# Kernel tuning notes

Measured on AMD Instinct MI355X. Metric: run time of the kernel, lower is better.

Reference implementation:

```python
import jax, jax.numpy as jnp
import numpy as np

B, T = 64, 2048
QD, KD, VD, AD = 512, 512, 512, 256


def setup_inputs() -> dict:
    key = jax.random.key(0)
    ks = jax.random.split(key, 9)
    s = lambda d: 1.0 / np.sqrt(d)
    return {
        "query": jax.random.normal(ks[0], (B, QD), jnp.float32),
        "key": jax.random.normal(ks[1], (B, T, KD), jnp.float32),
        "value": jax.random.normal(ks[2], (B, T, VD), jnp.float32),
        "Wq": jax.random.uniform(ks[3], (QD, AD), jnp.float32, -s(QD), s(QD)),
        "bq": jax.random.uniform(ks[4], (AD,), jnp.float32, -s(QD), s(QD)),
        "Wk": jax.random.uniform(ks[5], (KD, AD), jnp.float32, -s(KD), s(KD)),
        "bk": jax.random.uniform(ks[6], (AD,), jnp.float32, -s(KD), s(KD)),
        "Wo": jax.random.uniform(ks[7], (AD, 1), jnp.float32, -s(AD), s(AD)),
        "bo": jax.random.uniform(ks[8], (1,), jnp.float32, -s(AD), s(AD)),
    }


def reference(query, key, value, Wq, bq, Wk, bk, Wo, bo):
    # q_proj: [B, 1, AD]; k_proj: [B, T, AD]
    q_proj = (query @ Wq + bq)[:, None, :]
    k_proj = jnp.einsum("btk,ka->bta", key, Wk) + bk
    # score: [B, T, 1]
    score = jnp.tanh(q_proj + k_proj) @ Wo + bo
    attn = jax.nn.softmax(score, axis=1)  # softmax over keys (dim 1)
    # context: [B, VD] = sum_t attn[b,t] * value[b,t,:]
    context = jnp.einsum("bt,btv->bv", attn[..., 0], value)
    return context, attn[..., 0]
```

## Files before the change

### kernel.cpp

```cpp
#include <hip/hip_runtime.h>

#define NB 64
#define NT 2048
#define NQD 512
#define NKD 512
#define NVD 512
#define NAD 256

typedef __attribute__((ext_vector_type(8))) short s16x8;
typedef __attribute__((ext_vector_type(4))) float fx4;
typedef __attribute__((ext_vector_type(4))) unsigned int u32x4;

__device__ __forceinline__ short f2bf(float x) {
  union { float f; unsigned u; } v; v.f = x;
  return (short)((v.u + 0x7fffu + ((v.u >> 16) & 1u)) >> 16);
}

__device__ __forceinline__ unsigned cvt_pk_bf16(float lo, float hi) {
  unsigned r;
  asm("v_cvt_pk_bf16_f32 %0, %1, %2" : "=v"(r) : "v"(lo), "v"(hi));
  return r;
}

__device__ __forceinline__ float fast_tanh(float x) {
  float e = __expf(x + x);
  return 1.0f - 2.0f * __builtin_amdgcn_rcpf(e + 1.0f);
}

__device__ __forceinline__ void gload_lds16(const void* g, void* l) {
  __builtin_amdgcn_global_load_lds(
      (const __attribute__((address_space(1))) unsigned int*)g,
      (__attribute__((address_space(3))) unsigned int*)l, 16, 0, 0);
}

__global__ void prep_kernel(const float* __restrict__ query, const float* __restrict__ Wq,
                            const float* __restrict__ bq, const float* __restrict__ bk,
                            const float* __restrict__ Wk,
                            float* __restrict__ qpk, short* __restrict__ Bpk) {
  __shared__ float q[NQD];
  const int tid = threadIdx.x;
  if (blockIdx.x < NB) {
    const int b = blockIdx.x;
    for (int k = tid; k < NQD; k += 256) q[k] = query[b * NQD + k];
    __syncthreads();
    float acc = bq[tid] + bk[tid];
#pragma unroll 8
    for (int k = 0; k < NQD; ++k) acc += q[k] * Wq[k * NAD + tid];
    qpk[b * NAD + tid] = acc;
  } else {
    const int ks = blockIdx.x - NB;
#pragma unroll
    for (int rep = 0; rep < 4; ++rep) {
      const int o = rep * 256 + tid;
      const int wnt = o >> 6;
      const int l = o & 63;
      const int g = l >> 4, h = l & 15;
      const int n = wnt * 16 + h;
      const int k0 = ks * 32 + g * 8;
      s16x8 v;
#pragma unroll
      for (int j = 0; j < 8; ++j) v[j] = f2bf(Wk[(size_t)(k0 + j) * NAD + n]);
      *(s16x8*)(Bpk + (size_t)(ks * 1024 + o) * 8) = v;
    }
  }
}

__global__ void __launch_bounds__(512, 4)
score_kernel(const float* __restrict__ key, const short* __restrict__ Bpk,
             const float* __restrict__ qpk, const float* __restrict__ Wo,
             float* __restrict__ score) {
  __shared__ float As[2][128 * 32];
  __shared__ short Bs[2][256 * 32];
  __shared__ float sred[4][128];
  const int tid = threadIdx.x;
  const int W = tid >> 6, l = tid & 63;
  const int wr = W >> 2, wc = W & 3;
  const int g = l >> 4, h = l & 15;
  const int m0 = blockIdx.x * 128;
  const int b = m0 >> 11;

  const float* srcA[2];
  int loffA[2];
#pragma unroll
  for (int i = 0; i < 2; ++i) {
    const int p = W * 128 + i * 64 + l;
    const int row = p >> 3, c = p & 7;
    srcA[i] = key + (size_t)(m0 + row) * NKD + ((c ^ (row & 7)) << 2);
    loffA[i] = (W * 128 + i * 64) * 16;
  }
  const short* srcB[2];
  int loffB[2];
#pragma unroll
  for (int i = 0; i < 2; ++i) {
    const int o = W * 128 + i * 64 + l;
    srcB[i] = Bpk + (size_t)o * 8;
    loffB[i] = (W * 128 + i * 64) * 16;
  }

  auto stage = [&](int bb, int ck) {
#pragma unroll
    for (int i = 0; i < 2; ++i)
      gload_lds16(srcA[i] + ck * 32, (char*)&As[bb][0] + loffA[i]);
#pragma unroll
    for (int i = 0; i < 2; ++i)
      gload_lds16(srcB[i] + (size_t)ck * 8192, (char*)&Bs[bb][0] + loffB[i]);
  };

  stage(0, 0);
  stage(1, 1);

  fx4 acc[4][4];
#pragma unroll
  for (int i = 0; i < 4; ++i)
#pragma unroll
    for (int j = 0; j < 4; ++j) acc[i][j] = fx4{0.f, 0.f, 0.f, 0.f};

  for (int ck = 0; ck < 16; ++ck) {
    const int buf = ck & 1;
    if (ck < 15) asm volatile("s_waitcnt vmcnt(4)" ::: "memory");
    else         asm volatile("s_waitcnt vmcnt(0)" ::: "memory");
    __builtin_amdgcn_sched_barrier(0);
    __builtin_amdgcn_s_barrier();

    s16x8 bfr[4];
#pragma unroll
    for (int nt = 0; nt < 4; ++nt)
      bfr[nt] = *(const s16x8*)((const char*)&Bs[buf][0] + ((wc * 4 + nt) * 64 + l) * 16);
#pragma unroll
    for (int mt = 0; mt < 4; ++mt) {
      const int R = wr * 64 + mt * 16 + h;
      const char* base = (const char*)&As[buf][0] + R * 128;
      fx4 lo = *(const fx4*)(base + (((g * 2    ) ^ (R & 7)) << 4));
      fx4 hi = *(const fx4*)(base + (((g * 2 + 1) ^ (R & 7)) << 4));
      u32x4 uu;
      uu[0] = cvt_pk_bf16(lo[0], lo[1]);
      uu[1] = cvt_pk_bf16(lo[2], lo[3]);
      uu[2] = cvt_pk_bf16(hi[0], hi[1]);
      uu[3] = cvt_pk_bf16(hi[2], hi[3]);
      const s16x8 af = *(s16x8*)&uu;
#pragma unroll
      for (int nt = 0; nt < 4; ++nt)
        acc[mt][nt] = __builtin_amdgcn_mfma_f32_16x16x32_bf16(af, bfr[nt], acc[mt][nt], 0, 0, 0);
    }

    __builtin_amdgcn_s_barrier();
    if (ck < 14) stage(buf, ck + 2);
  }

  float qv[4], wv[4];
#pragma unroll
  for (int nt = 0; nt < 4; ++nt) {
    const int n = wc * 64 + nt * 16 + h;
    qv[nt] = qpk[b * NAD + n];
    wv[nt] = Wo[n];
  }
#pragma unroll
  for (int mt = 0; mt < 4; ++mt) {
#pragma unroll
    for (int rr = 0; rr < 4; ++rr) {
      float s = fast_tanh(acc[mt][0][rr] + qv[0]) * wv[0]
              + fast_tanh(acc[mt][1][rr] + qv[1]) * wv[1]
              + fast_tanh(acc[mt][2][rr] + qv[2]) * wv[2]
              + fast_tanh(acc[mt][3][rr] + qv[3]) * wv[3];
#pragma unroll
      for (int off = 1; off < 16; off <<= 1) s += __shfl_xor(s, off, 64);
      if (h == 0) sred[wc][wr * 64 + mt * 16 + g * 4 + rr] = s;
    }
  }
  __syncthreads();
  if (tid < 128)
    score[m0 + tid] = sred[0][tid] + sred[1][tid] + sred[2][tid] + sred[3][tid];
}

__global__ void ctx_sm_kernel(const float* __restrict__ score, const float* __restrict__ value,
                              float* __restrict__ attn, float* __restrict__ partial) {
  __shared__ float pa[NT];
  __shared__ float redm[4];
  __shared__ float reds[4];
  __shared__ fx4 red[128];
  const int blk = blockIdx.x;
  const int b = blk >> 5, tc = blk & 31;
  const int tid = threadIdx.x;

  const float* s = score + (size_t)b * NT;
  float v[8];
  float m = -3.0e38f;
#pragma unroll
  for (int j = 0; j < 8; ++j) { v[j] = s[tid + j * 256]; m = fmaxf(m, v[j]); }
#pragma unroll
  for (int off = 1; off < 64; off <<= 1) m = fmaxf(m, __shfl_xor(m, off, 64));
  if ((tid & 63) == 0) redm[tid >> 6] = m;
  __syncthreads();
  m = fmaxf(fmaxf(redm[0], redm[1]), fmaxf(redm[2], redm[3]));
  float sum = 0.f;
#pragma unroll
  for (int j = 0; j < 8; ++j) { v[j] = __expf(v[j] - m); sum += v[j]; }
#pragma unroll
  for (int off = 1; off < 64; off <<= 1) sum += __shfl_xor(sum, off, 64);
  if ((tid & 63) == 0) reds[tid >> 6] = sum;
  __syncthreads();
  sum = reds[0] + reds[1] + reds[2] + reds[3];
  const float inv = 1.0f / sum;
#pragma unroll
  for (int j = 0; j < 8; ++j) pa[tid + j * 256] = v[j] * inv;
  __syncthreads();

  if (tid < 64) attn[(size_t)b * NT + tc * 64 + tid] = pa[tc * 64 + tid];

  const float* a = &pa[tc * 64];
  const int half = tid >> 7;
  const int vi = (tid & 127) * 4;
  const float* vp = value + ((size_t)b * NT + tc * 64 + half) * NVD + vi;
  fx4 s4 = fx4{0.f, 0.f, 0.f, 0.f};
#pragma unroll 8
  for (int t = 0; t < 64; t += 2) {
    fx4 x = *(const fx4*)(vp + (size_t)t * NVD);
    s4 += x * a[t + half];
  }
  if (half) red[tid & 127] = s4;
  __syncthreads();
  if (!half) {
    s4 += red[tid];
    *(fx4*)(partial + (size_t)blk * NVD + vi) = s4;
  }
}

__global__ void ctx_reduce_kernel(const float* __restrict__ partial, float* __restrict__ ctx) {
  const int i = blockIdx.x * 256 + threadIdx.x;
  const int b = i >> 9, v = i & (NVD - 1);
  float s = 0.f;
#pragma unroll
  for (int tc = 0; tc < 32; ++tc) s += partial[(size_t)(b * 32 + tc) * NVD + v];
  ctx[i] = s;
}

extern "C" void kernel_launch(void* const* d_in, const int* in_sizes, int n_in,
                              void* d_out, int out_size, void* d_ws, size_t ws_size,
                              hipStream_t stream) {
  const float* query = (const float*)d_in[0];
  const float* key   = (const float*)d_in[1];
  const float* value = (const float*)d_in[2];
  const float* Wq    = (const float*)d_in[3];
  const float* bq    = (const float*)d_in[4];
  const float* Wk    = (const float*)d_in[5];
  const float* bk    = (const float*)d_in[6];
  const float* Wo    = (const float*)d_in[7];

  float* out  = (float*)d_out;
  float* ctx  = out;
  float* attn = out + NB * NVD;

  char* ws = (char*)d_ws;
  float* qpk     = (float*)(ws);
  short* Bpk     = (short*)(ws + 64 * 1024);
  float* score   = (float*)(ws + (64 + 256) * 1024);
  float* partial = (float*)(ws + (64 + 256 + 512) * 1024);

  prep_kernel<<<NB + 16, 256, 0, stream>>>(query, Wq, bq, bk, Wk, qpk, Bpk);
  score_kernel<<<(NB * NT) / 128, 512, 0, stream>>>(key, Bpk, qpk, Wo, score);
  ctx_sm_kernel<<<NB * 32, 256, 0, stream>>>(score, value, attn, partial);
  ctx_reduce_kernel<<<(NB * NVD) / 256, 256, 0, stream>>>(partial, ctx);
}
```

Measured before the change: 150.8 us.

## Split score GEMM columns across two smaller blocks with partial score buffers

The score kernel goes from 128x256 tiles on 512 threads to 64x128 tiles on 256 threads. Each pair of blocks covers the two column halves of the attention dimension, and each half writes its partial score to its own buffer. The softmax kernel sums the two partial buffers when it loads scores. This raises block count and should ease register and LDS pressure per block, but each key row is now loaded twice (by the two column-half blocks), relying on L2 to absorb the duplicate traffic.

```diff
diff --git a/kernel.cpp b/kernel.cpp
--- a/kernel.cpp
+++ b/kernel.cpp
@@ -65,18 +65,19 @@
   }
 }
 
-__global__ void __launch_bounds__(512, 4)
+__global__ void __launch_bounds__(256, 4)
 score_kernel(const float* __restrict__ key, const short* __restrict__ Bpk,
              const float* __restrict__ qpk, const float* __restrict__ Wo,
-             float* __restrict__ score) {
-  __shared__ float As[2][128 * 32];
-  __shared__ short Bs[2][256 * 32];
-  __shared__ float sred[4][128];
+             float* __restrict__ score0, float* __restrict__ score1) {
+  __shared__ float As[2][64 * 32];
+  __shared__ short Bs[2][128 * 32];
+  __shared__ float sred[4][64];
   const int tid = threadIdx.x;
   const int W = tid >> 6, l = tid & 63;
-  const int wr = W >> 2, wc = W & 3;
   const int g = l >> 4, h = l & 15;
-  const int m0 = blockIdx.x * 128;
+  const int bm = blockIdx.x >> 1;
+  const int bc = blockIdx.x & 1;
+  const int m0 = bm * 64;
   const int b = m0 >> 11;
 
   const float* srcA[2];
@@ -93,7 +94,7 @@
 #pragma unroll
   for (int i = 0; i < 2; ++i) {
     const int o = W * 128 + i * 64 + l;
-    srcB[i] = Bpk + (size_t)o * 8;
+    srcB[i] = Bpk + (size_t)bc * 4096 + (size_t)o * 8;
     loffB[i] = (W * 128 + i * 64) * 16;
   }
 
@@ -109,11 +110,11 @@
   stage(0, 0);
   stage(1, 1);
 
-  fx4 acc[4][4];
+  fx4 acc[4][2];
 #pragma unroll
   for (int i = 0; i < 4; ++i)
 #pragma unroll
-    for (int j = 0; j < 4; ++j) acc[i][j] = fx4{0.f, 0.f, 0.f, 0.f};
+    for (int j = 0; j < 2; ++j) acc[i][j] = fx4{0.f, 0.f, 0.f, 0.f};
 
   for (int ck = 0; ck < 16; ++ck) {
     const int buf = ck & 1;
@@ -122,13 +123,13 @@
     __builtin_amdgcn_sched_barrier(0);
     __builtin_amdgcn_s_barrier();
 
-    s16x8 bfr[4];
-#pragma unroll
-    for (int nt = 0; nt < 4; ++nt)
-      bfr[nt] = *(const s16x8*)((const char*)&Bs[buf][0] + ((wc * 4 + nt) * 64 + l) * 16);
+    s16x8 bfr[2];
+#pragma unroll
+    for (int nt = 0; nt < 2; ++nt)
+      bfr[nt] = *(const s16x8*)((const char*)&Bs[buf][0] + ((W * 2 + nt) * 64 + l) * 16);
 #pragma unroll
     for (int mt = 0; mt < 4; ++mt) {
-      const int R = wr * 64 + mt * 16 + h;
+      const int R = mt * 16 + h;
       const char* base = (const char*)&As[buf][0] + R * 128;
       fx4 lo = *(const fx4*)(base + (((g * 2    ) ^ (R & 7)) << 4));
       fx4 hi = *(const fx4*)(base + (((g * 2 + 1) ^ (R & 7)) << 4));
@@ -139,7 +140,7 @@
       uu[3] = cvt_pk_bf16(hi[2], hi[3]);
       const s16x8 af = *(s16x8*)&uu;
 #pragma unroll
-      for (int nt = 0; nt < 4; ++nt)
+      for (int nt = 0; nt < 2; ++nt)
         acc[mt][nt] = __builtin_amdgcn_mfma_f32_16x16x32_bf16(af, bfr[nt], acc[mt][nt], 0, 0, 0);
     }
 
@@ -147,10 +148,10 @@
     if (ck < 14) stage(buf, ck + 2);
   }
 
-  float qv[4], wv[4];
-#pragma unroll
-  for (int nt = 0; nt < 4; ++nt) {
-    const int n = wc * 64 + nt * 16 + h;
+  float qv[2], wv[2];
+#pragma unroll
+  for (int nt = 0; nt < 2; ++nt) {
+    const int n = bc * 128 + W * 32 + nt * 16 + h;
     qv[nt] = qpk[b * NAD + n];
     wv[nt] = Wo[n];
   }
@@ -159,20 +160,21 @@
 #pragma unroll
     for (int rr = 0; rr < 4; ++rr) {
       float s = fast_tanh(acc[mt][0][rr] + qv[0]) * wv[0]
-              + fast_tanh(acc[mt][1][rr] + qv[1]) * wv[1]
-              + fast_tanh(acc[mt][2][rr] + qv[2]) * wv[2]
-              + fast_tanh(acc[mt][3][rr] + qv[3]) * wv[3];
+              + fast_tanh(acc[mt][1][rr] + qv[1]) * wv[1];
 #pragma unroll
       for (int off = 1; off < 16; off <<= 1) s += __shfl_xor(s, off, 64);
-      if (h == 0) sred[wc][wr * 64 + mt * 16 + g * 4 + rr] = s;
+      if (h == 0) sred[W][mt * 16 + g * 4 + rr] = s;
     }
   }
   __syncthreads();
-  if (tid < 128)
-    score[m0 + tid] = sred[0][tid] + sred[1][tid] + sred[2][tid] + sred[3][tid];
-}
-
-__global__ void ctx_sm_kernel(const float* __restrict__ score, const float* __restrict__ value,
+  if (tid < 64) {
+    float* dst = bc ? score1 : score0;
+    dst[m0 + tid] = sred[0][tid] + sred[1][tid] + sred[2][tid] + sred[3][tid];
+  }
+}
+
+__global__ void ctx_sm_kernel(const float* __restrict__ score0, const float* __restrict__ score1,
+                              const float* __restrict__ value,
                               float* __restrict__ attn, float* __restrict__ partial) {
   __shared__ float pa[NT];
   __shared__ float redm[4];
@@ -182,11 +184,15 @@
   const int b = blk >> 5, tc = blk & 31;
   const int tid = threadIdx.x;
 
-  const float* s = score + (size_t)b * NT;
+  const float* s0 = score0 + (size_t)b * NT;
+  const float* s1 = score1 + (size_t)b * NT;
   float v[8];
   float m = -3.0e38f;
 #pragma unroll
-  for (int j = 0; j < 8; ++j) { v[j] = s[tid + j * 256]; m = fmaxf(m, v[j]); }
+  for (int j = 0; j < 8; ++j) {
+    v[j] = s0[tid + j * 256] + s1[tid + j * 256];
+    m = fmaxf(m, v[j]);
+  }
 #pragma unroll
   for (int off = 1; off < 64; off <<= 1) m = fmaxf(m, __shfl_xor(m, off, 64));
   if ((tid & 63) == 0) redm[tid >> 6] = m;
@@ -253,11 +259,12 @@
   char* ws = (char*)d_ws;
   float* qpk     = (float*)(ws);
   short* Bpk     = (short*)(ws + 64 * 1024);
-  float* score   = (float*)(ws + (64 + 256) * 1024);
-  float* partial = (float*)(ws + (64 + 256 + 512) * 1024);
+  float* score0  = (float*)(ws + (64 + 256) * 1024);
+  float* score1  = (float*)(ws + (64 + 256 + 512) * 1024);
+  float* partial = (float*)(ws + (64 + 256 + 1024) * 1024);
 
   prep_kernel<<<NB + 16, 256, 0, stream>>>(query, Wq, bq, bk, Wk, qpk, Bpk);
-  score_kernel<<<(NB * NT) / 128, 512, 0, stream>>>(key, Bpk, qpk, Wo, score);
-  ctx_sm_kernel<<<NB * 32, 256, 0, stream>>>(score, value, attn, partial);
+  score_kernel<<<(NB * NT) / 64 * 2, 256, 0, stream>>>(key, Bpk, qpk, Wo, score0, score1);
+  ctx_sm_kernel<<<NB * 32, 256, 0, stream>>>(score0, score1, value, attn, partial);
   ctx_reduce_kernel<<<(NB * NVD) / 256, 256, 0, stream>>>(partial, ctx);
 }
```

Result: slower. 184.3 us (+22.2%).

## Fuse score and softmax-context kernels with per-batch atomic grid barrier

Applied to the files above, without the earlier changes.

Merges the score GEMM kernel and the softmax/context kernel into one persistent-style kernel of 512 blocks. Each block handles two 128-row tiles, then blocks of the same batch synchronize through an atomic counter spin-wait before computing softmax and four context chunks each. This removes one kernel launch and the gap between them, and may let value reads overlap other batches' GEMM work. In exchange it relies on all 8 blocks of a batch being co-resident, since otherwise the spin-wait can deadlock. It also adds a memset and puts more work in each block.

```diff
diff --git a/kernel.cpp b/kernel.cpp
--- a/kernel.cpp
+++ b/kernel.cpp
@@ -66,162 +66,182 @@
 }
 
 __global__ void __launch_bounds__(512, 4)
-score_kernel(const float* __restrict__ key, const short* __restrict__ Bpk,
-             const float* __restrict__ qpk, const float* __restrict__ Wo,
-             float* __restrict__ score) {
-  __shared__ float As[2][128 * 32];
-  __shared__ short Bs[2][256 * 32];
-  __shared__ float sred[4][128];
+merged_kernel(const float* __restrict__ key, const short* __restrict__ Bpk,
+              const float* __restrict__ qpk, const float* __restrict__ Wo,
+              const float* __restrict__ value,
+              float* __restrict__ score, float* __restrict__ attn,
+              float* __restrict__ partial, int* __restrict__ cnt) {
+  __shared__ __align__(16) char smem[67584];
   const int tid = threadIdx.x;
   const int W = tid >> 6, l = tid & 63;
   const int wr = W >> 2, wc = W & 3;
   const int g = l >> 4, h = l & 15;
-  const int m0 = blockIdx.x * 128;
-  const int b = m0 >> 11;
-
-  const float* srcA[2];
-  int loffA[2];
-#pragma unroll
-  for (int i = 0; i < 2; ++i) {
-    const int p = W * 128 + i * 64 + l;
-    const int row = p >> 3, c = p & 7;
-    srcA[i] = key + (size_t)(m0 + row) * NKD + ((c ^ (row & 7)) << 2);
-    loffA[i] = (W * 128 + i * 64) * 16;
-  }
-  const short* srcB[2];
-  int loffB[2];
-#pragma unroll
-  for (int i = 0; i < 2; ++i) {
-    const int o = W * 128 + i * 64 + l;
-    srcB[i] = Bpk + (size_t)o * 8;
-    loffB[i] = (W * 128 + i * 64) * 16;
-  }
-
-  auto stage = [&](int bb, int ck) {
-#pragma unroll
-    for (int i = 0; i < 2; ++i)
-      gload_lds16(srcA[i] + ck * 32, (char*)&As[bb][0] + loffA[i]);
-#pragma unroll
-    for (int i = 0; i < 2; ++i)
-      gload_lds16(srcB[i] + (size_t)ck * 8192, (char*)&Bs[bb][0] + loffB[i]);
-  };
-
-  stage(0, 0);
-  stage(1, 1);
-
-  fx4 acc[4][4];
-#pragma unroll
-  for (int i = 0; i < 4; ++i)
-#pragma unroll
-    for (int j = 0; j < 4; ++j) acc[i][j] = fx4{0.f, 0.f, 0.f, 0.f};
-
-  for (int ck = 0; ck < 16; ++ck) {
-    const int buf = ck & 1;
-    if (ck < 15) asm volatile("s_waitcnt vmcnt(4)" ::: "memory");
-    else         asm volatile("s_waitcnt vmcnt(0)" ::: "memory");
-    __builtin_amdgcn_sched_barrier(0);
-    __builtin_amdgcn_s_barrier();
-
-    s16x8 bfr[4];
-#pragma unroll
-    for (int nt = 0; nt < 4; ++nt)
-      bfr[nt] = *(const s16x8*)((const char*)&Bs[buf][0] + ((wc * 4 + nt) * 64 + l) * 16);
+  const int b = blockIdx.x >> 3;
+  const int j = blockIdx.x & 7;
+
+  for (int st = 0; st < 2; ++st) {
+    const int m0 = (blockIdx.x * 2 + st) * 128;
+    char* AsB = smem;
+    char* BsB = smem + 32768;
+    float* sred = (float*)(smem + 65536);
+
+    const float* srcA[2];
+    int loffA[2];
+#pragma unroll
+    for (int i = 0; i < 2; ++i) {
+      const int p = W * 128 + i * 64 + l;
+      const int row = p >> 3, c = p & 7;
+      srcA[i] = key + (size_t)(m0 + row) * NKD + ((c ^ (row & 7)) << 2);
+      loffA[i] = (W * 128 + i * 64) * 16;
+    }
+    const short* srcB[2];
+    int loffB[2];
+#pragma unroll
+    for (int i = 0; i < 2; ++i) {
+      const int o = W * 128 + i * 64 + l;
+      srcB[i] = Bpk + (size_t)o * 8;
+      loffB[i] = (W * 128 + i * 64) * 16;
+    }
+
+    auto stage = [&](int bb, int ck) {
+#pragma unroll
+      for (int i = 0; i < 2; ++i)
+        gload_lds16(srcA[i] + ck * 32, AsB + bb * 16384 + loffA[i]);
+#pragma unroll
+      for (int i = 0; i < 2; ++i)
+        gload_lds16(srcB[i] + (size_t)ck * 8192, BsB + bb * 16384 + loffB[i]);
+    };
+
+    stage(0, 0);
+    stage(1, 1);
+
+    fx4 acc[4][4];
+#pragma unroll
+    for (int i = 0; i < 4; ++i)
+#pragma unroll
+      for (int jj = 0; jj < 4; ++jj) acc[i][jj] = fx4{0.f, 0.f, 0.f, 0.f};
+
+    for (int ck = 0; ck < 16; ++ck) {
+      const int buf = ck & 1;
+      if (ck < 15) asm volatile("s_waitcnt vmcnt(4)" ::: "memory");
+      else         asm volatile("s_waitcnt vmcnt(0)" ::: "memory");
+      __builtin_amdgcn_sched_barrier(0);
+      __builtin_amdgcn_s_barrier();
+
+      s16x8 bfr[4];
+#pragma unroll
+      for (int nt = 0; nt < 4; ++nt)
+        bfr[nt] = *(const s16x8*)(BsB + buf * 16384 + ((wc * 4 + nt) * 64 + l) * 16);
+#pragma unroll
+      for (int mt = 0; mt < 4; ++mt) {
+        const int R = wr * 64 + mt * 16 + h;
+        const char* base = AsB + buf * 16384 + R * 128;
+        fx4 lo = *(const fx4*)(base + (((g * 2    ) ^ (R & 7)) << 4));
+        fx4 hi = *(const fx4*)(base + (((g * 2 + 1) ^ (R & 7)) << 4));
+        u32x4 uu;
+        uu[0] = cvt_pk_bf16(lo[0], lo[1]);
+        uu[1] = cvt_pk_bf16(lo[2], lo[3]);
+        uu[2] = cvt_pk_bf16(hi[0], hi[1]);
+        uu[3] = cvt_pk_bf16(hi[2], hi[3]);
+        const s16x8 af = *(s16x8*)&uu;
+#pragma unroll
+        for (int nt = 0; nt < 4; ++nt)
+          acc[mt][nt] = __builtin_amdgcn_mfma_f32_16x16x32_bf16(af, bfr[nt], acc[mt][nt], 0, 0, 0);
+      }
+
+      __builtin_amdgcn_s_barrier();
+      if (ck < 14) stage(buf, ck + 2);
+    }
+
+    float qv[4], wv[4];
+#pragma unroll
+    for (int nt = 0; nt < 4; ++nt) {
+      const int n = wc * 64 + nt * 16 + h;
+      qv[nt] = qpk[b * NAD + n];
+      wv[nt] = Wo[n];
+    }
 #pragma unroll
     for (int mt = 0; mt < 4; ++mt) {
-      const int R = wr * 64 + mt * 16 + h;
-      const char* base = (const char*)&As[buf][0] + R * 128;
-      fx4 lo = *(const fx4*)(base + (((g * 2    ) ^ (R & 7)) << 4));
-      fx4 hi = *(const fx4*)(base + (((g * 2 + 1) ^ (R & 7)) << 4));
-      u32x4 uu;
-      uu[0] = cvt_pk_bf16(lo[0], lo[1]);
-      uu[1] = cvt_pk_bf16(lo[2], lo[3]);
-      uu[2] = cvt_pk_bf16(hi[0], hi[1]);
-      uu[3] = cvt_pk_bf16(hi[2], hi[3]);
-      const s16x8 af = *(s16x8*)&uu;
-#pragma unroll
-      for (int nt = 0; nt < 4; ++nt)
-        acc[mt][nt] = __builtin_amdgcn_mfma_f32_16x16x32_bf16(af, bfr[nt], acc[mt][nt], 0, 0, 0);
-    }
-
-    __builtin_amdgcn_s_barrier();
-    if (ck < 14) stage(buf, ck + 2);
-  }
-
-  float qv[4], wv[4];
-#pragma unroll
-  for (int nt = 0; nt < 4; ++nt) {
-    const int n = wc * 64 + nt * 16 + h;
-    qv[nt] = qpk[b * NAD + n];
-    wv[nt] = Wo[n];
-  }
-#pragma unroll
-  for (int mt = 0; mt < 4; ++mt) {
-#pragma unroll
-    for (int rr = 0; rr < 4; ++rr) {
-      float s = fast_tanh(acc[mt][0][rr] + qv[0]) * wv[0]
-              + fast_tanh(acc[mt][1][rr] + qv[1]) * wv[1]
-              + fast_tanh(acc[mt][2][rr] + qv[2]) * wv[2]
-              + fast_tanh(acc[mt][3][rr] + qv[3]) * wv[3];
-#pragma unroll
-      for (int off = 1; off < 16; off <<= 1) s += __shfl_xor(s, off, 64);
-      if (h == 0) sred[wc][wr * 64 + mt * 16 + g * 4 + rr] = s;
-    }
+#pragma unroll
+      for (int rr = 0; rr < 4; ++rr) {
+        float s = fast_tanh(acc[mt][0][rr] + qv[0]) * wv[0]
+                + fast_tanh(acc[mt][1][rr] + qv[1]) * wv[1]
+                + fast_tanh(acc[mt][2][rr] + qv[2]) * wv[2]
+                + fast_tanh(acc[mt][3][rr] + qv[3]) * wv[3];
+#pragma unroll
+        for (int off = 1; off < 16; off <<= 1) s += __shfl_xor(s, off, 64);
+        if (h == 0) sred[wc * 128 + (wr << 6) + mt * 16 + g * 4 + rr] = s;
+      }
+    }
+    __syncthreads();
+    if (tid < 128)
+      score[m0 + tid] = sred[0 * 128 + tid] + sred[1 * 128 + tid] +
+                        sred[2 * 128 + tid] + sred[3 * 128 + tid];
+    __syncthreads();
+  }
+
+  __threadfence();
+  if (tid == 0) {
+    atomicAdd(&cnt[b], 1);
+    while (atomicAdd(&cnt[b], 0) < 8) __builtin_amdgcn_s_sleep(8);
   }
   __syncthreads();
-  if (tid < 128)
-    score[m0 + tid] = sred[0][tid] + sred[1][tid] + sred[2][tid] + sred[3][tid];
-}
-
-__global__ void ctx_sm_kernel(const float* __restrict__ score, const float* __restrict__ value,
-                              float* __restrict__ attn, float* __restrict__ partial) {
-  __shared__ float pa[NT];
-  __shared__ float redm[4];
-  __shared__ float reds[4];
-  __shared__ fx4 red[128];
-  const int blk = blockIdx.x;
-  const int b = blk >> 5, tc = blk & 31;
-  const int tid = threadIdx.x;
-
-  const float* s = score + (size_t)b * NT;
-  float v[8];
-  float m = -3.0e38f;
-#pragma unroll
-  for (int j = 0; j < 8; ++j) { v[j] = s[tid + j * 256]; m = fmaxf(m, v[j]); }
-#pragma unroll
-  for (int off = 1; off < 64; off <<= 1) m = fmaxf(m, __shfl_xor(m, off, 64));
-  if ((tid & 63) == 0) redm[tid >> 6] = m;
-  __syncthreads();
-  m = fmaxf(fmaxf(redm[0], redm[1]), fmaxf(redm[2], redm[3]));
-  float sum = 0.f;
-#pragma unroll
-  for (int j = 0; j < 8; ++j) { v[j] = __expf(v[j] - m); sum += v[j]; }
-#pragma unroll
-  for (int off = 1; off < 64; off <<= 1) sum += __shfl_xor(sum, off, 64);
-  if ((tid & 63) == 0) reds[tid >> 6] = sum;
-  __syncthreads();
-  sum = reds[0] + reds[1] + reds[2] + reds[3];
-  const float inv = 1.0f / sum;
-#pragma unroll
-  for (int j = 0; j < 8; ++j) pa[tid + j * 256] = v[j] * inv;
-  __syncthreads();
-
-  if (tid < 64) attn[(size_t)b * NT + tc * 64 + tid] = pa[tc * 64 + tid];
-
-  const float* a = &pa[tc * 64];
-  const int half = tid >> 7;
-  const int vi = (tid & 127) * 4;
-  const float* vp = value + ((size_t)b * NT + tc * 64 + half) * NVD + vi;
-  fx4 s4 = fx4{0.f, 0.f, 0.f, 0.f};
-#pragma unroll 8
-  for (int t = 0; t < 64; t += 2) {
-    fx4 x = *(const fx4*)(vp + (size_t)t * NVD);
-    s4 += x * a[t + half];
-  }
-  if (half) red[tid & 127] = s4;
-  __syncthreads();
-  if (!half) {
-    s4 += red[tid];
-    *(fx4*)(partial + (size_t)blk * NVD + vi) = s4;
+  __threadfence();
+
+  float* pa = (float*)smem;
+  float* redm = (float*)(smem + 8192);
+  float* reds = (float*)(smem + 8224);
+  fx4* red = (fx4*)(smem + 8256);
+  {
+    const float* s = score + (size_t)b * NT;
+    float v[4];
+    float m = -3.0e38f;
+#pragma unroll
+    for (int q4 = 0; q4 < 4; ++q4) { v[q4] = s[tid + q4 * 512]; m = fmaxf(m, v[q4]); }
+#pragma unroll
+    for (int off = 1; off < 64; off <<= 1) m = fmaxf(m, __shfl_xor(m, off, 64));
+    if (l == 0) redm[W] = m;
+    __syncthreads();
+#pragma unroll
+    for (int k = 0; k < 8; ++k) m = fmaxf(m, redm[k]);
+    float sum = 0.f;
+#pragma unroll
+    for (int q4 = 0; q4 < 4; ++q4) { v[q4] = __expf(v[q4] - m); sum += v[q4]; }
+#pragma unroll
+    for (int off = 1; off < 64; off <<= 1) sum += __shfl_xor(sum, off, 64);
+    if (l == 0) reds[W] = sum;
+    __syncthreads();
+    sum = 0.f;
+#pragma unroll
+    for (int k = 0; k < 8; ++k) sum += reds[k];
+    const float inv = 1.0f / sum;
+#pragma unroll
+    for (int q4 = 0; q4 < 4; ++q4) pa[tid + q4 * 512] = v[q4] * inv;
+    __syncthreads();
+  }
+
+  const int rg = tid >> 7, cs = tid & 127;
+#pragma unroll 1
+  for (int c = 0; c < 4; ++c) {
+    const int cidx = j * 4 + c;
+    if (tid < 64) attn[(size_t)b * NT + cidx * 64 + tid] = pa[cidx * 64 + tid];
+    const float* vp = value + ((size_t)b * NT + cidx * 64 + rg) * NVD + cs * 4;
+    const float* a = &pa[cidx * 64 + rg];
+    fx4 s4 = fx4{0.f, 0.f, 0.f, 0.f};
+#pragma unroll 4
+    for (int t = 0; t < 16; ++t) {
+      fx4 x = *(const fx4*)(vp + (size_t)t * 4 * NVD);
+      s4 += x * a[t * 4];
+    }
+    if (rg) red[(rg - 1) * 128 + cs] = s4;
+    __syncthreads();
+    if (rg == 0) {
+      s4 += red[0 * 128 + cs];
+      s4 += red[1 * 128 + cs];
+      s4 += red[2 * 128 + cs];
+      *(fx4*)(partial + (size_t)(b * 32 + cidx) * NVD + cs * 4) = s4;
+    }
+    __syncthreads();
   }
 }
 
@@ -255,9 +275,11 @@
   short* Bpk     = (short*)(ws + 64 * 1024);
   float* score   = (float*)(ws + (64 + 256) * 1024);
   float* partial = (float*)(ws + (64 + 256 + 512) * 1024);
-
+  int*   cnt     = (int*)(ws + (64 + 256 + 512) * 1024 + 4 * 1024 * 1024);
+
+  (void)hipMemsetAsync(cnt, 0, NB * sizeof(int), stream);
   prep_kernel<<<NB + 16, 256, 0, stream>>>(query, Wq, bq, bk, Wk, qpk, Bpk);
-  score_kernel<<<(NB * NT) / 128, 512, 0, stream>>>(key, Bpk, qpk, Wo, score);
-  ctx_sm_kernel<<<NB * 32, 256, 0, stream>>>(score, value, attn, partial);
+  merged_kernel<<<512, 512, 0, stream>>>(key, Bpk, qpk, Wo, value,
+                                         score, attn, partial, cnt);
   ctx_reduce_kernel<<<(NB * NVD) / 256, 256, 0, stream>>>(partial, ctx);
 }
```

Result: slower. 452.0 us (+199.8%).
